# Kernel optimization log

Hardware: AMD Instinct MI355X
Metric: run time of the kernel (lower is better)

## Reference

```python
import jax, jax.numpy as jnp
import numpy as np

N = 10000          # nodes
E = 200000         # edges (avg degree 20)
LAT = 128          # latent dim
NEXP = 8           # experts
NTYPE = 95         # atom types (hard-coded 95x0e in module)
M0, M1, M2 = 128, 64, 32          # node/out irreps muls for l=0,1,2 (dim 480)
E0, E1, E2 = 64, 32, 16           # edge irreps muls (dim 240)
C0, C1, C2 = M0 + E0, M1 + E1, M2 + E2   # concat channels per l
T0 = M0 + M1 + M2                 # gate-input scalars: 128 scalars + 96 gates
AVG_NEIGH = 20.0


def setup_inputs() -> dict:
    key = jax.random.key(0)
    ks = jax.random.split(key, 32)
    r = lambda i, sh: jax.random.normal(ks[i], sh, dtype=jnp.float32)
    return {
        "latents": r(0, (E, LAT)),
        "node_features": r(1, (N, M0 + 3 * M1 + 5 * M2)),
        "edge_features": r(2, (E, E0 + 3 * E1 + 5 * E2)),
        "edge_vector": r(3, (E, 3)),
        "mole_globals": r(4, (LAT,)),
        "wigner_D1": r(5, (E, 3, 3)),
        "wigner_D2": r(6, (E, 5, 5)),
        "node_onehot": jax.nn.one_hot(jax.random.randint(ks[7], (N,), 0, NTYPE), NTYPE, dtype=jnp.float32),
        "Wg": r(8, (LAT, NEXP)),
        "Wm": r(9, (LAT, NEXP)),
        "W0_e": r(10, (NEXP, C0, T0)), "W0_s": r(11, (C0, T0)),
        "W1_e": r(12, (NEXP, C1, M1)), "W1_s": r(13, (C1, M1)),
        "W2_e": r(14, (NEXP, C2, M2)), "W2_s": r(15, (C2, M2)),
        "Wp0": r(16, (M0, M0)), "bp0": jnp.zeros((M0,), jnp.float32),
        "Wp1": r(17, (M1, M1)), "Wp2": r(18, (M2, M2)),
        "Wenv": r(19, (LAT, M0 + M1 + M2)),
        "Woh0": r(20, (M0, NTYPE)), "Woh1": r(21, (M1, NTYPE)), "Woh2": r(22, (M2, NTYPE)),
        "atom_type": jax.random.randint(ks[23], (N,), 0, NTYPE),
        "edge_index": jax.random.randint(ks[24], (2, E), 0, N),
        "active_edges": jnp.arange(E),
    }


def _mix(x, We, Ws, g):
    """Latent(expert)-conditioned per-l channel mixing: y = x @ (sum_e g_e W_e + W_shared).
    Loops over the small fixed expert count; never materializes per-edge weight matrices."""
    xm = x if x.ndim == 3 else x[:, :, None]           # [a, c, m]
    y = jnp.einsum('acm,co->aom', xm, Ws)
    for e in range(NEXP):
        y = y + g[:, e, None, None] * jnp.einsum('acm,co->aom', xm, We[e])
    y = y * float(1.0 / np.sqrt(xm.shape[1]))
    return y[:, :, 0] if x.ndim == 2 else y


def reference(latents, node_features, edge_features, edge_vector, mole_globals,
              wigner_D1, wigner_D2, node_onehot, Wg, Wm,
              W0_e, W0_s, W1_e, W1_s, W2_e, W2_s,
              Wp0, bp0, Wp1, Wp2, Wenv, Woh0, Woh1, Woh2,
              atom_type, edge_index, active_edges):
    edge_center = edge_index[0][active_edges]
    lat = latents[active_edges]
    # gather node features along edges, split irreps blocks
    xn = node_features[edge_center]                         # [Ea, 480]
    n0 = xn[:, :M0]
    n1 = xn[:, M0:M0 + 3 * M1].reshape(-1, M1, 3)
    n2 = xn[:, M0 + 3 * M1:].reshape(-1, M2, 5)
    e0 = edge_features[:, :E0]
    e1 = edge_features[:, E0:E0 + 3 * E1].reshape(-1, E1, 3)
    e2 = edge_features[:, E0 + 3 * E1:].reshape(-1, E2, 5)
    x0 = jnp.concatenate([n0, e0], axis=1)                  # [Ea, C0]
    x1 = jnp.concatenate([n1, e1], axis=1)                  # [Ea, C1, 3]
    x2 = jnp.concatenate([n2, e2], axis=1)                  # [Ea, C2, 5]
    # latent + molecular-global conditioned expert gates
    gates = jax.nn.softmax(lat @ Wg + mole_globals @ Wm, axis=-1)   # [Ea, NEXP]
    # SO(2)-style TP: rotate l>0 blocks into edge frame (Wigner-D), mix channels, rotate back
    x1r = jnp.einsum('amn,acn->acm', wigner_D1, x1)
    x2r = jnp.einsum('amn,acn->acm', wigner_D2, x2)
    t0 = _mix(x0, W0_e, W0_s, gates)                        # [Ea, T0]
    t1 = jnp.einsum('anm,aom->aon', wigner_D1, _mix(x1r, W1_e, W1_s, gates))
    t2 = jnp.einsum('anm,aom->aon', wigner_D2, _mix(x2r, W2_e, W2_s, gates))
    # Gate nonlinearity: silu scalars, sigmoid gates scale l>0 channels
    s = jax.nn.silu(t0[:, :M0])
    v1 = t1 * jax.nn.sigmoid(t0[:, M0:M0 + M1])[:, :, None]
    v2 = t2 * jax.nn.sigmoid(t0[:, M0 + M1:])[:, :, None]
    # lin_post: per-l equivariant linear (bias only on scalars), fan-in normalized
    s = s @ Wp0 * float(1.0 / np.sqrt(M0)) + bp0
    v1 = jnp.einsum('acm,co->aom', v1, Wp1) * float(1.0 / np.sqrt(M1))
    v2 = jnp.einsum('acm,co->aom', v2, Wp2) * float(1.0 / np.sqrt(M2))
    # E3ElementLinear: per-channel weights generated from latents
    w = lat @ Wenv * float(1.0 / np.sqrt(LAT))              # [Ea, M0+M1+M2]
    s = s * w[:, :M0]
    v1 = v1 * w[:, M0:M0 + M1, None]
    v2 = v2 * w[:, M0 + M1:, None]
    # scatter-reduce messages to nodes, normalize by rsqrt(avg_num_neighbors)
    norm = float(1.0 / np.sqrt(AVG_NEIGH))
    o0 = jax.ops.segment_sum(s, edge_center, num_segments=N) * norm
    o1 = jax.ops.segment_sum(v1, edge_center, num_segments=N) * norm
    o2 = jax.ops.segment_sum(v2, edge_center, num_segments=N) * norm
    # residual blend (res_update_params=0 -> u=sigmoid(0)=0.5), identity residual
    u = 0.5
    c_old = float(1.0 / np.sqrt(u * u + 1.0))
    c_new = u * c_old
    h0 = c_old * node_features[:, :M0] + c_new * o0
    h1 = c_old * node_features[:, M0:M0 + 3 * M1].reshape(N, M1, 3) + c_new * o1
    h2 = c_old * node_features[:, M0 + 3 * M1:].reshape(N, M2, 5) + c_new * o2
    # layer-onehot 'uvu' weighted TP with 95x0e, fan-in normalized, added residually
    invs = float(1.0 / np.sqrt(NTYPE))
    h0 = h0 + h0 * (node_onehot @ Woh0.T) * invs
    h1 = h1 + h1 * (node_onehot @ Woh1.T)[:, :, None] * invs
    h2 = h2 + h2 * (node_onehot @ Woh2.T)[:, :, None] * invs
    return jnp.concatenate([h0, h1.reshape(N, 3 * M1), h2.reshape(N, 5 * M2)], axis=1)
```

## Files before the change

### kernel.cpp

```cpp
#include <hip/hip_runtime.h>
#include <math.h>

namespace {

typedef __attribute__((ext_vector_type(8))) short short8;
typedef __attribute__((ext_vector_type(4))) float f32x4;

constexpr int kN   = 10000;
constexpr int kE   = 200000;
constexpr int kNT  = 95;
constexpr int kNFD = 480;

__device__ __forceinline__ ushort bf(float f) {
  union { float f; uint u; } c; c.f = f;
  uint r = c.u + 0x7FFF + ((c.u >> 16) & 1);
  return (ushort)(r >> 16);
}
__device__ __forceinline__ float fb(ushort u) {
  union { uint u; float f; } c; c.u = ((uint)u) << 16;
  return c.f;
}
__device__ __forceinline__ uint pk2(float a, float b) {
  return (uint)bf(a) | ((uint)bf(b) << 16);
}

__device__ __forceinline__ void packone(int u, const float* We, const float* Ws,
                                        int expStride, int Kreal, int Nstride,
                                        int Nreal, int NT, int NKp, ushort* d) {
  int i = u & 7;
  int lane = (u >> 3) & 63;
  int rest = u >> 9;
  int kc = rest % NKp; rest /= NKp;
  int nt = rest % NT;
  int e  = rest / NT;
  int k = kc*32 + (lane >> 4)*8 + i;
  int n = nt*16 + (lane & 15);
  float v = 0.f;
  if (k < Kreal && n < Nreal) {
    const float* s = (Ws != nullptr && e == 8) ? Ws : (We + (size_t)e*expStride);
    v = s[(size_t)k*Nstride + n];
  }
  d[u] = bf(v);
}

constexpr int PK0   = 0;
constexpr int PK1   = 442368;
constexpr int PK2   = 497664;
constexpr int PKENV = 516096;
constexpr int PKP0  = 544768;
constexpr int PKP1  = 561152;
constexpr int PKP2  = 565248;
constexpr int PKTOT = 566272;

__global__ __launch_bounds__(256)
void pack_k(const float* __restrict__ W0e, const float* __restrict__ W0s,
            const float* __restrict__ W1e, const float* __restrict__ W1s,
            const float* __restrict__ W2e, const float* __restrict__ W2s,
            const float* __restrict__ Wenv, const float* __restrict__ Wp0,
            const float* __restrict__ Wp1, const float* __restrict__ Wp2,
            ushort* __restrict__ dst) {
  int gid = blockIdx.x*256 + threadIdx.x;
  if (gid >= PKTOT) return;
  if (gid < PK1)        packone(gid - PK0,   W0e, W0s, 192*224, 192, 224, 224, 16, 6, dst + PK0);
  else if (gid < PK2)   packone(gid - PK1,   W1e, W1s, 96*64,    96,  64,  64,  4, 3, dst + PK1);
  else if (gid < PKENV) packone(gid - PK2,   W2e, W2s, 48*32,    48,  32,  32,  2, 2, dst + PK2);
  else if (gid < PKP0)  packone(gid - PKENV, Wenv, nullptr, 0,  128, 224, 224, 14, 4, dst + PKENV);
  else if (gid < PKP1)  packone(gid - PKP0,  Wp0, nullptr, 0,   128, 128, 128,  8, 4, dst + PKP0);
  else if (gid < PKP2)  packone(gid - PKP1,  Wp1, nullptr, 0,    64,  64,  64,  4, 2, dst + PKP1);
  else                  packone(gid - PKP2,  Wp2, nullptr, 0,    32,  32,  32,  2, 1, dst + PKP2);
}

__global__ __launch_bounds__(64)
void mgl_k(const float* __restrict__ mgv, const float* __restrict__ Wm,
           float* __restrict__ mgl) {
  int x = threadIdx.x;
  if (x < 8) {
    float s = 0.f;
    for (int l = 0; l < 128; ++l) s += mgv[l]*Wm[l*8 + x];
    mgl[x] = s;
  }
}

__global__ __launch_bounds__(256)
void hist_k(const int* __restrict__ eidx, const int* __restrict__ act,
            int* __restrict__ counts) {
  int e = blockIdx.x*256 + threadIdx.x;
  if (e < kE) atomicAdd(&counts[eidx[act[e]]], 1);
}

__global__ __launch_bounds__(256)
void scan_k(const int* __restrict__ counts, int* __restrict__ rowptr,
            int* __restrict__ cursor) {
  __shared__ int part[256];
  const int t = threadIdx.x;
  const int start = t*40;
  int local = 0;
  for (int i = 0; i < 40; ++i) {
    int idx = start + i;
    if (idx < kN) local += counts[idx];
  }
  part[t] = local;
  __syncthreads();
  for (int ofs = 1; ofs < 256; ofs <<= 1) {
    int v = (t >= ofs) ? part[t - ofs] : 0;
    __syncthreads();
    part[t] += v;
    __syncthreads();
  }
  int run = part[t] - local;
  for (int i = 0; i < 40; ++i) {
    int idx = start + i;
    if (idx < kN) {
      rowptr[idx] = run;
      cursor[idx] = run;
      run += counts[idx];
    }
  }
  if (t == 255) rowptr[kN] = run;
}

__global__ __launch_bounds__(256)
void scatter_k(const int* __restrict__ eidx, const int* __restrict__ act,
               int* __restrict__ cursor, int* __restrict__ elist) {
  int e = blockIdx.x*256 + threadIdx.x;
  if (e < kE) {
    int n = eidx[act[e]];
    int pos = atomicAdd(&cursor[n], 1);
    elist[pos] = e;
  }
}

__global__ __launch_bounds__(256)
void prep_k(const float* __restrict__ latents, const float* __restrict__ nodef,
            const float* __restrict__ edgef, const float* __restrict__ mgl,
            const float* __restrict__ D1, const float* __restrict__ D2,
            const float* __restrict__ Wg,
            const int* __restrict__ eidx, const int* __restrict__ act,
            float* __restrict__ coefg,
            ushort* __restrict__ x0, ushort* __restrict__ x1r,
            ushort* __restrict__ x2r) {
  __shared__ int aidl[32], cenl[32];
  const int tid = threadIdx.x;
  const int base = blockIdx.x*32;

  if (tid < 32) {
    int a = act[base + tid];
    aidl[tid] = a;
    cenl[tid] = eidx[a];
  }
  __syncthreads();

  {
    int e = tid >> 3, x = tid & 7;
    const float* lat = latents + (size_t)aidl[e]*128;
    float s = mgl[x];
    for (int l = 0; l < 128; ++l) s += lat[l]*Wg[l*8 + x];
    float mx = s;
    mx = fmaxf(mx, __shfl_xor(mx, 1));
    mx = fmaxf(mx, __shfl_xor(mx, 2));
    mx = fmaxf(mx, __shfl_xor(mx, 4));
    float ex = __expf(s - mx);
    float sm = ex;
    sm += __shfl_xor(sm, 1);
    sm += __shfl_xor(sm, 2);
    sm += __shfl_xor(sm, 4);
    size_t a = base + e;
    coefg[a*9 + x] = ex/sm;
    if (x == 0) coefg[a*9 + 8] = 1.f;
  }

  for (int u = tid; u < 32*24; u += 256) {
    int e = u/24, g = u - e*24;
    int c0 = g*8;
    size_t a = base + e;
    const float* s = (g < 16) ? (nodef + (size_t)cenl[e]*kNFD + c0)
                              : (edgef + a*240 + (c0 - 128));
    float4 f0 = *(const float4*)s;
    float4 f1 = *(const float4*)(s + 4);
    uint4 o;
    o.x = pk2(f0.x, f0.y); o.y = pk2(f0.z, f0.w);
    o.z = pk2(f1.x, f1.y); o.w = pk2(f1.z, f1.w);
    *(uint4*)(x0 + a*192 + c0) = o;
  }

  for (int u = tid; u < 32*36; u += 256) {
    int e = u/36, r = u - e*36;
    int mm = r/12, g = r - mm*12;
    int c0 = g*8;
    size_t a = base + e;
    const float* dd = D1 + a*9 + mm*3;
    const float* s = (g < 8) ? (nodef + (size_t)cenl[e]*kNFD + 128 + c0*3)
                             : (edgef + a*240 + 64 + (c0 - 64)*3);
    float ld[24];
    #pragma unroll
    for (int q = 0; q < 6; ++q)
      *(float4*)(ld + q*4) = *(const float4*)(s + q*4);
    float d0 = dd[0], d1 = dd[1], d2 = dd[2];
    float ov[8];
    #pragma unroll
    for (int j = 0; j < 8; ++j)
      ov[j] = d0*ld[3*j] + d1*ld[3*j + 1] + d2*ld[3*j + 2];
    uint4 o;
    o.x = pk2(ov[0], ov[1]); o.y = pk2(ov[2], ov[3]);
    o.z = pk2(ov[4], ov[5]); o.w = pk2(ov[6], ov[7]);
    *(uint4*)(x1r + (a*3 + mm)*96 + c0) = o;
  }

  for (int u = tid; u < 32*40; u += 256) {
    int e = u/40, r = u - e*40;
    int mm = r >> 3, g = r & 7;
    int c0 = g*8;
    size_t a = base + e;
    uint4 o = {0u,0u,0u,0u};
    if (g < 6) {
      const float* dd = D2 + a*25 + mm*5;
      const float* s = (g < 4) ? (nodef + (size_t)cenl[e]*kNFD + 320 + c0*5)
                               : (edgef + a*240 + 160 + (c0 - 32)*5);
      float ld[40];
      #pragma unroll
      for (int q = 0; q < 10; ++q)
        *(float4*)(ld + q*4) = *(const float4*)(s + q*4);
      float d0 = dd[0], d1 = dd[1], d2 = dd[2], d3 = dd[3], d4 = dd[4];
      float ov[8];
      #pragma unroll
      for (int j = 0; j < 8; ++j)
        ov[j] = d0*ld[5*j] + d1*ld[5*j+1] + d2*ld[5*j+2] + d3*ld[5*j+3] + d4*ld[5*j+4];
      o.x = pk2(ov[0], ov[1]); o.y = pk2(ov[2], ov[3]);
      o.z = pk2(ov[4], ov[5]); o.w = pk2(ov[6], ov[7]);
    }
    *(uint4*)(x2r + (a*5 + mm)*64 + c0) = o;
  }
}

constexpr int gemm_smbytes(int K1, int NK, int N, int NEXP) {
  int LDA = K1 + 8;
  int NT = N/16;
  int a = 128*LDA*2;
  int b = NT*NK*1024;
  int u = a > b ? a : b;
  return u + (NEXP > 1 ? 128*NEXP*4 : 0);
}

template<int DIV, int K1, int NK, int N, int NEXP, int EPI, bool AF32>
__global__ __launch_bounds__(512)
void gemm_k(const ushort* __restrict__ A, const float* __restrict__ Af,
            const int* __restrict__ ridx, int strideA,
            const ushort* __restrict__ Bpk, const float* __restrict__ coefg,
            int rowsReal, float norm,
            ushort* __restrict__ outbf, const float* __restrict__ bias,
            const ushort* __restrict__ wenvbf, int WCOL) {
  constexpr int NT  = N/16;
  constexpr int CTW = NT/2;
  constexpr int LDA = K1 + 8;
  constexpr int ABYTES = 128*LDA*2;
  constexpr int BBYTES = NT*NK*1024;
  constexpr int UNI = (ABYTES > BBYTES) ? ABYTES : BBYTES;

  extern __shared__ char smraw[];
  ushort* Asm = (ushort*)smraw;
  float* coefsm = (float*)(smraw + UNI);

  const int tid = threadIdx.x;
  const int row0 = blockIdx.x*128;

  constexpr int C8 = K1/8;
  for (int u = tid; u < 128*C8; u += 512) {
    int r = u / C8, c8 = u - r*C8;
    int gr = row0 + r;
    uint4 v = {0u,0u,0u,0u};
    if (gr < rowsReal) {
      if constexpr (AF32) {
        const float* s = Af + (size_t)(ridx ? ridx[gr] : gr)*strideA + c8*8;
        float4 f0 = *(const float4*)s;
        float4 f1 = *(const float4*)(s + 4);
        v.x = pk2(f0.x, f0.y); v.y = pk2(f0.z, f0.w);
        v.z = pk2(f1.x, f1.y); v.w = pk2(f1.z, f1.w);
      } else {
        v = *(const uint4*)(A + (size_t)gr*strideA + c8*8);
      }
    }
    *(uint4*)(&Asm[r*LDA + c8*8]) = v;
  }
  if constexpr (NEXP > 1) {
    for (int u = tid; u < 128*NEXP; u += 512) {
      int r = u / NEXP, e = u - r*NEXP;
      int a = (row0 + r)/DIV;
      coefsm[r*NEXP + e] = coefg[(size_t)a*NEXP + e];
    }
  }
  __syncthreads();

  const int lane = tid & 63, wid = tid >> 6;
  const int cg = wid & 1, rg = wid >> 1;
  const int rbase = rg*32;
  const int lrow = lane & 15, lkb = lane >> 4;

  short8 af[2][NK];
  #pragma unroll
  for (int rt = 0; rt < 2; ++rt)
    #pragma unroll
    for (int kc = 0; kc < NK; ++kc)
      af[rt][kc] = *(const short8*)(&Asm[(rbase + rt*16 + lrow)*LDA + kc*32 + lkb*8]);

  f32x4 acc[2][CTW];
  #pragma unroll
  for (int rt = 0; rt < 2; ++rt)
    #pragma unroll
    for (int ct = 0; ct < CTW; ++ct)
      acc[rt][ct] = f32x4{0.f,0.f,0.f,0.f};

  __syncthreads();

  union BU { uint4 u; short8 s; };
  uint4* Bsm4 = (uint4*)smraw;
  const uint4* Bg4 = (const uint4*)Bpk;

  for (int e = 0; e < NEXP; ++e) {
    for (int u = tid; u < NT*NK*64; u += 512)
      Bsm4[u] = Bg4[(size_t)e*(NT*NK*64) + u];
    __syncthreads();

    if constexpr (NEXP > 1) {
      float cf[2][4];
      #pragma unroll
      for (int rt = 0; rt < 2; ++rt)
        #pragma unroll
        for (int q = 0; q < 4; ++q)
          cf[rt][q] = coefsm[(rbase + rt*16 + lkb*4 + q)*NEXP + e];
      #pragma unroll
      for (int ct = 0; ct < CTW; ++ct) {
        int nt = cg*CTW + ct;
        f32x4 z[2];
        z[0] = f32x4{0.f,0.f,0.f,0.f};
        z[1] = f32x4{0.f,0.f,0.f,0.f};
        #pragma unroll
        for (int kc = 0; kc < NK; ++kc) {
          BU b; b.u = Bsm4[(nt*NK + kc)*64 + lane];
          z[0] = __builtin_amdgcn_mfma_f32_16x16x32_bf16(af[0][kc], b.s, z[0], 0, 0, 0);
          z[1] = __builtin_amdgcn_mfma_f32_16x16x32_bf16(af[1][kc], b.s, z[1], 0, 0, 0);
        }
        #pragma unroll
        for (int q = 0; q < 4; ++q) {
          acc[0][ct][q] += cf[0][q]*z[0][q];
          acc[1][ct][q] += cf[1][q]*z[1][q];
        }
      }
    } else {
      #pragma unroll
      for (int ct = 0; ct < CTW; ++ct) {
        int nt = cg*CTW + ct;
        #pragma unroll
        for (int kc = 0; kc < NK; ++kc) {
          BU b; b.u = Bsm4[(nt*NK + kc)*64 + lane];
          acc[0][ct] = __builtin_amdgcn_mfma_f32_16x16x32_bf16(af[0][kc], b.s, acc[0][ct], 0, 0, 0);
          acc[1][ct] = __builtin_amdgcn_mfma_f32_16x16x32_bf16(af[1][kc], b.s, acc[1][ct], 0, 0, 0);
        }
      }
    }
    __syncthreads();
  }

  #pragma unroll
  for (int rt = 0; rt < 2; ++rt) {
    #pragma unroll
    for (int ct = 0; ct < CTW; ++ct) {
      #pragma unroll
      for (int q = 0; q < 4; ++q) {
        int gr = row0 + rbase + rt*16 + lkb*4 + q;
        if (gr >= rowsReal) continue;
        int o = (cg*CTW + ct)*16 + lrow;
        float val = acc[rt][ct][q]*norm;
        if constexpr (EPI == 0) {
          outbf[(size_t)gr*N + o] = bf(val);
        } else if constexpr (EPI == 1) {
          float av = (o < 128) ? (val/(1.f + __expf(-val)))
                               : (1.f/(1.f + __expf(-val)));
          outbf[(size_t)gr*N + o] = bf(av);
        } else {
          int a = gr/DIV;
          if (bias != nullptr) val += bias[o];
          float w = fb(wenvbf[(size_t)a*224 + WCOL + o]);
          val *= w*0.22360679774997896f;
          outbf[(size_t)gr*N + o] = bf(val);
        }
      }
    }
  }
}

constexpr int T0SMB = 55808;

template<int C>
__device__ __forceinline__ void t0_phase(int e, int tid, int lane, int cg,
                                         int rbase, int lkb,
                                         const short8 (&af)[2][6],
                                         f32x4 (&acc)[2][7],
                                         const float* coefsm,
                                         uint4* Bsm4, const uint4* Bg4,
                                         uint4& rg0, uint4& rg1, uint4& rg2) {
  __syncthreads();
  const bool hasNext = !(e == 8 && C == 3);
  if (hasNext) {
    int ne = e + (C == 3 ? 1 : 0);
    int nc = (C + 1) & 3;
    const uint4* s = Bg4 + (size_t)ne*6144 + (size_t)nc*1536;
    rg0 = s[tid]; rg1 = s[tid + 512]; rg2 = s[tid + 1024];
  }
  float cf[2][4];
  #pragma unroll
  for (int rt = 0; rt < 2; ++rt)
    #pragma unroll
    for (int q = 0; q < 4; ++q)
      cf[rt][q] = coefsm[(rbase + rt*16 + lkb*4 + q)*9 + e];
  union BU { uint4 u; short8 s; };
  const uint4* bb = Bsm4 + (C & 1)*1536;
  {
    f32x4 z0 = {0.f,0.f,0.f,0.f}, z1 = {0.f,0.f,0.f,0.f};
    #pragma unroll
    for (int kc = 0; kc < 6; ++kc) {
      BU b; b.u = bb[(cg*6 + kc)*64 + lane];
      z0 = __builtin_amdgcn_mfma_f32_16x16x32_bf16(af[0][kc], b.s, z0, 0, 0, 0);
      z1 = __builtin_amdgcn_mfma_f32_16x16x32_bf16(af[1][kc], b.s, z1, 0, 0, 0);
    }
    #pragma unroll
    for (int q = 0; q < 4; ++q) {
      acc[0][2*C][q] += cf[0][q]*z0[q];
      acc[1][2*C][q] += cf[1][q]*z1[q];
    }
  }
  if constexpr (2*C + 1 < 7) {
    f32x4 z0 = {0.f,0.f,0.f,0.f}, z1 = {0.f,0.f,0.f,0.f};
    #pragma unroll
    for (int kc = 0; kc < 6; ++kc) {
      BU b; b.u = bb[((2 + cg)*6 + kc)*64 + lane];
      z0 = __builtin_amdgcn_mfma_f32_16x16x32_bf16(af[0][kc], b.s, z0, 0, 0, 0);
      z1 = __builtin_amdgcn_mfma_f32_16x16x32_bf16(af[1][kc], b.s, z1, 0, 0, 0);
    }
    #pragma unroll
    for (int q = 0; q < 4; ++q) {
      acc[0][2*C + 1][q] += cf[0][q]*z0[q];
      acc[1][2*C + 1][q] += cf[1][q]*z1[q];
    }
  }
  __syncthreads();
  if (hasNext) {
    uint4* d = Bsm4 + ((C + 1) & 1)*1536;
    d[tid] = rg0; d[tid + 512] = rg1; d[tid + 1024] = rg2;
  }
}

__global__ __launch_bounds__(512, 2)
void t0c_k(const ushort* __restrict__ A, const ushort* __restrict__ Bpk,
           const float* __restrict__ coefg, ushort* __restrict__ outbf) {
  extern __shared__ char smraw[];
  ushort* Asm = (ushort*)smraw;
  float* coefsm = (float*)(smraw + 51200);
  uint4* Bsm4 = (uint4*)smraw;
  const uint4* Bg4 = (const uint4*)Bpk;

  const int tid = threadIdx.x;
  const int row0 = blockIdx.x*128;

  for (int u = tid; u < 128*24; u += 512) {
    int r = u/24, c8 = u - r*24;
    int gr = row0 + r;
    uint4 v = {0u,0u,0u,0u};
    if (gr < kE) v = *(const uint4*)(A + (size_t)gr*192 + c8*8);
    *(uint4*)(&Asm[r*200 + c8*8]) = v;
  }
  for (int u = tid; u < 128*9; u += 512) {
    int r = u/9, e = u - r*9;
    coefsm[r*9 + e] = coefg[(size_t)(row0 + r)*9 + e];
  }
  __syncthreads();

  const int lane = tid & 63, wid = tid >> 6;
  const int cg = wid & 1, rg = wid >> 1;
  const int rbase = rg*32;
  const int lrow = lane & 15, lkb = lane >> 4;

  short8 af[2][6];
  #pragma unroll
  for (int rt = 0; rt < 2; ++rt)
    #pragma unroll
    for (int kc = 0; kc < 6; ++kc)
      af[rt][kc] = *(const short8*)(&Asm[(rbase + rt*16 + lrow)*200 + kc*32 + lkb*8]);

  f32x4 acc[2][7];
  #pragma unroll
  for (int rt = 0; rt < 2; ++rt)
    #pragma unroll
    for (int ct = 0; ct < 7; ++ct)
      acc[rt][ct] = f32x4{0.f,0.f,0.f,0.f};

  __syncthreads();

  uint4 rg0, rg1, rg2;
  { const uint4* s = Bg4; rg0 = s[tid]; rg1 = s[tid + 512]; rg2 = s[tid + 1024]; }
  { uint4* d = Bsm4;      d[tid] = rg0; d[tid + 512] = rg1; d[tid + 1024] = rg2; }

  for (int e = 0; e < 9; ++e) {
    t0_phase<0>(e, tid, lane, cg, rbase, lkb, af, acc, coefsm, Bsm4, Bg4, rg0, rg1, rg2);
    t0_phase<1>(e, tid, lane, cg, rbase, lkb, af, acc, coefsm, Bsm4, Bg4, rg0, rg1, rg2);
    t0_phase<2>(e, tid, lane, cg, rbase, lkb, af, acc, coefsm, Bsm4, Bg4, rg0, rg1, rg2);
    t0_phase<3>(e, tid, lane, cg, rbase, lkb, af, acc, coefsm, Bsm4, Bg4, rg0, rg1, rg2);
  }

  #pragma unroll
  for (int rt = 0; rt < 2; ++rt) {
    #pragma unroll
    for (int ct = 0; ct < 7; ++ct) {
      #pragma unroll
      for (int q = 0; q < 4; ++q) {
        int gr = row0 + rbase + rt*16 + lkb*4 + q;
        if (gr >= kE) continue;
        int o = (2*ct + cg)*16 + lrow;
        float val = acc[rt][ct][q]*0.07216878364870323f;
        float av = (o < 128) ? (val/(1.f + __expf(-val)))
                             : (1.f/(1.f + __expf(-val)));
        outbf[(size_t)gr*224 + o] = bf(av);
      }
    }
  }
}

__global__ __launch_bounds__(256)
void mid_k(const ushort* __restrict__ y1, const ushort* __restrict__ y2,
           const ushort* __restrict__ t0act, const float* __restrict__ D1,
           const float* __restrict__ D2, ushort* __restrict__ v1,
           ushort* __restrict__ v2) {
  const int base = blockIdx.x*64;
  const int tid = threadIdx.x;

  for (int u = tid; u < 64*24; u += 256) {
    int e = u/24, r = u - e*24;
    int n = r >> 3, g = r & 7;
    int c0 = g*8;
    size_t a = base + e;
    const float* dd = D1 + a*9 + n*3;
    float d0 = dd[0], d1 = dd[1], d2 = dd[2];
    short8 m0 = *(const short8*)(y1 + ((size_t)a*3 + 0)*64 + c0);
    short8 m1 = *(const short8*)(y1 + ((size_t)a*3 + 1)*64 + c0);
    short8 m2 = *(const short8*)(y1 + ((size_t)a*3 + 2)*64 + c0);
    short8 gt = *(const short8*)(t0act + a*224 + 128 + c0);
    float ov[8];
    #pragma unroll
    for (int j = 0; j < 8; ++j) {
      float s = d0*fb((ushort)m0[j]) + d1*fb((ushort)m1[j]) + d2*fb((ushort)m2[j]);
      ov[j] = s*fb((ushort)gt[j]);
    }
    uint4 o;
    o.x = pk2(ov[0], ov[1]); o.y = pk2(ov[2], ov[3]);
    o.z = pk2(ov[4], ov[5]); o.w = pk2(ov[6], ov[7]);
    *(uint4*)(v1 + ((size_t)a*3 + n)*64 + c0) = o;
  }

  for (int u = tid; u < 64*20; u += 256) {
    int e = u/20, r = u - e*20;
    int n = r >> 2, g = r & 3;
    int c0 = g*8;
    size_t a = base + e;
    const float* dd = D2 + a*25 + n*5;
    short8 m0 = *(const short8*)(y2 + ((size_t)a*5 + 0)*32 + c0);
    short8 m1 = *(const short8*)(y2 + ((size_t)a*5 + 1)*32 + c0);
    short8 m2 = *(const short8*)(y2 + ((size_t)a*5 + 2)*32 + c0);
    short8 m3 = *(const short8*)(y2 + ((size_t)a*5 + 3)*32 + c0);
    short8 m4 = *(const short8*)(y2 + ((size_t)a*5 + 4)*32 + c0);
    short8 gt = *(const short8*)(t0act + a*224 + 192 + c0);
    float ov[8];
    #pragma unroll
    for (int j = 0; j < 8; ++j) {
      float s = dd[0]*fb((ushort)m0[j]) + dd[1]*fb((ushort)m1[j])
              + dd[2]*fb((ushort)m2[j]) + dd[3]*fb((ushort)m3[j])
              + dd[4]*fb((ushort)m4[j]);
      ov[j] = s*fb((ushort)gt[j]);
    }
    uint4 o;
    o.x = pk2(ov[0], ov[1]); o.y = pk2(ov[2], ov[3]);
    o.z = pk2(ov[4], ov[5]); o.w = pk2(ov[6], ov[7]);
    *(uint4*)(v2 + ((size_t)a*5 + n)*32 + c0) = o;
  }
}

__global__ __launch_bounds__(256)
void gather_k(const float* __restrict__ nodef, const float* __restrict__ onehot,
              const float* __restrict__ Woh0, const float* __restrict__ Woh1,
              const float* __restrict__ Woh2,
              const int* __restrict__ rowptr, const int* __restrict__ elist,
              const ushort* __restrict__ pe0, const ushort* __restrict__ pe1,
              const ushort* __restrict__ pe2, float* __restrict__ out) {
  __shared__ int tn;
  const int n = blockIdx.x;
  const int t = threadIdx.x;
  if (t < kNT && onehot[(size_t)n*kNT + t] > 0.5f) tn = t;
  __syncthreads();
  const int ty = tn;
  const int r0 = rowptr[n], r1 = rowptr[n + 1];
  const float c_old = 0.8944271909999159f;
  const float c_new = 0.4472135954999579f;
  const float invs  = 0.10259783520851541f;

  for (int j = t; j < kNFD; j += 256) {
    int kind, row_m, col;
    if (j < 128)       { kind = 0; row_m = 0; col = j; }
    else if (j < 320)  { int jj = j - 128; col = jj/3; row_m = jj - col*3; kind = 1; }
    else               { int jj = j - 320; col = jj/5; row_m = jj - col*5; kind = 2; }

    float s = 0.f;
    for (int d = r0; d < r1; ++d) {
      int e = elist[d];
      ushort v;
      if (kind == 0)      v = pe0[(size_t)e*128 + col];
      else if (kind == 1) v = pe1[((size_t)e*3 + row_m)*64 + col];
      else                v = pe2[((size_t)e*5 + row_m)*32 + col];
      s += fb(v);
    }

    size_t idx = (size_t)n*kNFD + j;
    float h = c_old*nodef[idx] + c_new*s;
    float f;
    if (j < 128)      f = Woh0[j*kNT + ty];
    else if (j < 320) f = Woh1[((j - 128)/3)*kNT + ty];
    else              f = Woh2[((j - 320)/5)*kNT + ty];
    out[idx] = h*(1.f + f*invs);
  }
}

constexpr size_t OFF_CNT  = 0;
constexpr size_t OFF_CUR  = 40000;
constexpr size_t OFF_RP   = 80000;
constexpr size_t OFF_EL   = 120064;
constexpr size_t OFF_PACK = 1000000;
constexpr size_t OFF_COEF = 19200000;
constexpr size_t OFF_MGL  = 26402304;
constexpr size_t OFF_X0   = 27202560;
constexpr size_t OFF_X1R  = 104027136;
constexpr size_t OFF_X2R  = 219264000;
constexpr size_t OFF_WENV = 347272192;
constexpr size_t OFF_T0A  = 436900864;
constexpr size_t OFF_Y1   = 526529536;
constexpr size_t OFF_Y2   = 603354112;

}

extern "C" void kernel_launch(void* const* d_in, const int* in_sizes, int n_in,
                              void* d_out, int out_size, void* d_ws, size_t ws_size,
                              hipStream_t stream) {
  (void)in_sizes; (void)n_in; (void)out_size; (void)ws_size;
  const float* latents = (const float*)d_in[0];
  const float* nodef   = (const float*)d_in[1];
  const float* edgef   = (const float*)d_in[2];
  const float* mg      = (const float*)d_in[4];
  const float* D1      = (const float*)d_in[5];
  const float* D2      = (const float*)d_in[6];
  const float* onehot  = (const float*)d_in[7];
  const float* Wg      = (const float*)d_in[8];
  const float* Wm      = (const float*)d_in[9];
  const float* W0e     = (const float*)d_in[10];
  const float* W0s     = (const float*)d_in[11];
  const float* W1e     = (const float*)d_in[12];
  const float* W1s     = (const float*)d_in[13];
  const float* W2e     = (const float*)d_in[14];
  const float* W2s     = (const float*)d_in[15];
  const float* Wp0     = (const float*)d_in[16];
  const float* bp0     = (const float*)d_in[17];
  const float* Wp1     = (const float*)d_in[18];
  const float* Wp2     = (const float*)d_in[19];
  const float* Wenv    = (const float*)d_in[20];
  const float* Woh0    = (const float*)d_in[21];
  const float* Woh1    = (const float*)d_in[22];
  const float* Woh2    = (const float*)d_in[23];
  const int* eidx      = (const int*)d_in[25];
  const int* act       = (const int*)d_in[26];

  char* ws = (char*)d_ws;
  int*    cnt   = (int*)(ws + OFF_CNT);
  int*    cur   = (int*)(ws + OFF_CUR);
  int*    rp    = (int*)(ws + OFF_RP);
  int*    el    = (int*)(ws + OFF_EL);
  ushort* pk    = (ushort*)(ws + OFF_PACK);
  float*  coef  = (float*)(ws + OFF_COEF);
  float*  mgl   = (float*)(ws + OFF_MGL);
  ushort* x0    = (ushort*)(ws + OFF_X0);
  ushort* x1r   = (ushort*)(ws + OFF_X1R);
  ushort* x2r   = (ushort*)(ws + OFF_X2R);
  ushort* wenv  = (ushort*)(ws + OFF_WENV);
  ushort* t0act = (ushort*)(ws + OFF_T0A);
  ushort* y1    = (ushort*)(ws + OFF_Y1);
  ushort* y2    = (ushort*)(ws + OFF_Y2);
  ushort* v1    = (ushort*)(ws + OFF_X0);
  ushort* v2    = (ushort*)(ws + OFF_X1R);
  ushort* pe1   = (ushort*)(ws + OFF_X2R);
  ushort* pe2   = (ushort*)(ws + OFF_Y1);
  ushort* pe0   = (ushort*)(ws + OFF_Y2);
  float*  out   = (float*)d_out;

  hipMemsetAsync(cnt, 0, kN*sizeof(int), stream);
  hist_k<<<(kE + 255)/256, 256, 0, stream>>>(eidx, act, cnt);
  scan_k<<<1, 256, 0, stream>>>(cnt, rp, cur);
  scatter_k<<<(kE + 255)/256, 256, 0, stream>>>(eidx, act, cur, el);

  pack_k<<<(PKTOT + 255)/256, 256, 0, stream>>>(W0e, W0s, W1e, W1s, W2e, W2s,
                                                Wenv, Wp0, Wp1, Wp2, pk);
  mgl_k<<<1, 64, 0, stream>>>(mg, Wm, mgl);

  prep_k<<<kE/32, 256, 0, stream>>>(latents, nodef, edgef, mgl, D1, D2, Wg,
                                    eidx, act, coef, x0, x1r, x2r);

  {
    hipFuncSetAttribute((const void*)t0c_k,
                        hipFuncAttributeMaxDynamicSharedMemorySize, T0SMB);
    t0c_k<<<1563, 512, T0SMB, stream>>>(x0, pk + PK0, coef, t0act);
  }
  {
    auto kp = gemm_k<1,128,4,224,1,0,true>;
    int smb = gemm_smbytes(128,4,224,1);
    hipFuncSetAttribute((const void*)kp, hipFuncAttributeMaxDynamicSharedMemorySize, smb);
    kp<<<1563, 512, smb, stream>>>(
        nullptr, latents, act, 128, pk + PKENV, nullptr, kE, 0.08838834764831845f,
        wenv, nullptr, nullptr, 0);
  }
  {
    auto kp = gemm_k<3,96,3,64,9,0,false>;
    int smb = gemm_smbytes(96,3,64,9);
    hipFuncSetAttribute((const void*)kp, hipFuncAttributeMaxDynamicSharedMemorySize, smb);
    kp<<<4688, 512, smb, stream>>>(
        x1r, nullptr, nullptr, 96, pk + PK1, coef, 3*kE, 0.10206207261596577f,
        y1, nullptr, nullptr, 0);
  }
  {
    auto kp = gemm_k<5,64,2,32,9,0,false>;
    int smb = gemm_smbytes(64,2,32,9);
    hipFuncSetAttribute((const void*)kp, hipFuncAttributeMaxDynamicSharedMemorySize, smb);
    kp<<<7813, 512, smb, stream>>>(
        x2r, nullptr, nullptr, 64, pk + PK2, coef, 5*kE, 0.14433756729740643f,
        y2, nullptr, nullptr, 0);
  }

  mid_k<<<kE/64, 256, 0, stream>>>(y1, y2, t0act, D1, D2, v1, v2);

  {
    auto kp = gemm_k<1,128,4,128,1,2,false>;
    int smb = gemm_smbytes(128,4,128,1);
    hipFuncSetAttribute((const void*)kp, hipFuncAttributeMaxDynamicSharedMemorySize, smb);
    kp<<<1563, 512, smb, stream>>>(
        t0act, nullptr, nullptr, 224, pk + PKP0, nullptr, kE, 0.08838834764831845f,
        pe0, bp0, wenv, 0);
  }
  {
    auto kp = gemm_k<3,64,2,64,1,2,false>;
    int smb = gemm_smbytes(64,2,64,1);
    hipFuncSetAttribute((const void*)kp, hipFuncAttributeMaxDynamicSharedMemorySize, smb);
    kp<<<4688, 512, smb, stream>>>(
        v1, nullptr, nullptr, 64, pk + PKP1, nullptr, 3*kE, 0.125f,
        pe1, nullptr, wenv, 128);
  }
  {
    auto kp = gemm_k<5,32,1,32,1,2,false>;
    int smb = gemm_smbytes(32,1,32,1);
    hipFuncSetAttribute((const void*)kp, hipFuncAttributeMaxDynamicSharedMemorySize, smb);
    kp<<<7813, 512, smb, stream>>>(
        v2, nullptr, nullptr, 32, pk + PKP2, nullptr, 5*kE, 0.17677669529663687f,
        pe2, nullptr, wenv, 192);
  }

  gather_k<<<kN, 256, 0, stream>>>(nodef, onehot, Woh0, Woh1, Woh2,
                                   rp, el, pe0, pe1, pe2, out);
}
```

Measured before the change: 1.434 ms.

## Add dedicated double-buffered expert-mixing GEMM kernel for l=1,2 and lighter barriers

Replaces the generic gemm_k launches for the l=1 and l=2 expert-mixing GEMMs with a specialized kernel. It keeps A fragments in registers, streams each expert's packed weights through a double-buffered LDS with register prefetch, and accumulates coefficient-scaled MFMA results. It also swaps __syncthreads for a barrier that waits only on LDS counters (lgkmcnt) in both this kernel and the t0 kernel. The aim is to cut generic-kernel overhead and barrier stalls. The risk is that global prefetch loads are not covered by the barrier's wait.

```diff
diff --git a/kernel.cpp b/kernel.cpp
--- a/kernel.cpp
+++ b/kernel.cpp
@@ -22,6 +22,11 @@
 }
 __device__ __forceinline__ uint pk2(float a, float b) {
   return (uint)bf(a) | ((uint)bf(b) << 16);
+}
+
+__device__ __forceinline__ void fastbar() {
+  asm volatile("s_waitcnt lgkmcnt(0)" ::: "memory");
+  __builtin_amdgcn_s_barrier();
 }
 
 __device__ __forceinline__ void packone(int u, const float* We, const float* Ws,
@@ -398,7 +403,7 @@
                                          const float* coefsm,
                                          uint4* Bsm4, const uint4* Bg4,
                                          uint4& rg0, uint4& rg1, uint4& rg2) {
-  __syncthreads();
+  fastbar();
   const bool hasNext = !(e == 8 && C == 3);
   if (hasNext) {
     int ne = e + (C == 3 ? 1 : 0);
@@ -442,7 +447,7 @@
       acc[1][2*C + 1][q] += cf[1][q]*z1[q];
     }
   }
-  __syncthreads();
+  fastbar();
   if (hasNext) {
     uint4* d = Bsm4 + ((C + 1) & 1)*1536;
     d[tid] = rg0; d[tid + 512] = rg1; d[tid + 1024] = rg2;
@@ -519,6 +524,132 @@
         float av = (o < 128) ? (val/(1.f + __expf(-val)))
                              : (1.f/(1.f + __expf(-val)));
         outbf[(size_t)gr*224 + o] = bf(av);
+      }
+    }
+  }
+}
+
+constexpr int ych_smbytes(int K1, int NK, int NT) {
+  int a = 128*(K1 + 8)*2;
+  int b = 2*NT*NK*1024;
+  int u = a > b ? a : b;
+  return u + 128*9*4;
+}
+
+template<int DIV, int K1, int NK, int NT>
+__global__ __launch_bounds__(512, 2)
+void ychunk_k(const ushort* __restrict__ A, const ushort* __restrict__ Bpk,
+              const float* __restrict__ coefg, int rowsReal, float norm,
+              ushort* __restrict__ outbf) {
+  constexpr int CTW = NT/2;
+  constexpr int N   = NT*16;
+  constexpr int LDA = K1 + 8;
+  constexpr int ABYTES = 128*LDA*2;
+  constexpr int BBYTES = 2*NT*NK*1024;
+  constexpr int UNI = (ABYTES > BBYTES) ? ABYTES : BBYTES;
+  constexpr int NB4 = NT*NK*64;
+
+  extern __shared__ char smraw[];
+  ushort* Asm = (ushort*)smraw;
+  float* coefsm = (float*)(smraw + UNI);
+  uint4* Bsm4 = (uint4*)smraw;
+  const uint4* Bg4 = (const uint4*)Bpk;
+
+  const int tid = threadIdx.x;
+  const int row0 = blockIdx.x*128;
+
+  constexpr int C8 = K1/8;
+  for (int u = tid; u < 128*C8; u += 512) {
+    int r = u / C8, c8 = u - r*C8;
+    int gr = row0 + r;
+    uint4 v = {0u,0u,0u,0u};
+    if (gr < rowsReal) v = *(const uint4*)(A + (size_t)gr*K1 + c8*8);
+    *(uint4*)(&Asm[r*LDA + c8*8]) = v;
+  }
+  for (int u = tid; u < 128*9; u += 512) {
+    int r = u/9, e = u - r*9;
+    int a = (row0 + r)/DIV;
+    coefsm[r*9 + e] = coefg[(size_t)a*9 + e];
+  }
+  __syncthreads();
+
+  const int lane = tid & 63, wid = tid >> 6;
+  const int cg = wid & 1, rg = wid >> 1;
+  const int rbase = rg*32;
+  const int lrow = lane & 15, lkb = lane >> 4;
+
+  short8 af[2][NK];
+  #pragma unroll
+  for (int rt = 0; rt < 2; ++rt)
+    #pragma unroll
+    for (int kc = 0; kc < NK; ++kc)
+      af[rt][kc] = *(const short8*)(&Asm[(rbase + rt*16 + lrow)*LDA + kc*32 + lkb*8]);
+
+  f32x4 acc[2][CTW];
+  #pragma unroll
+  for (int rt = 0; rt < 2; ++rt)
+    #pragma unroll
+    for (int ct = 0; ct < CTW; ++ct)
+      acc[rt][ct] = f32x4{0.f,0.f,0.f,0.f};
+
+  __syncthreads();
+
+  union BU { uint4 u; short8 s; };
+  uint4 pf0, pf1;
+
+  if (tid < NB4) pf0 = Bg4[tid];
+  if constexpr (NB4 > 512) { if (tid + 512 < NB4) pf1 = Bg4[tid + 512]; }
+  if (tid < NB4) Bsm4[tid] = pf0;
+  if constexpr (NB4 > 512) { if (tid + 512 < NB4) Bsm4[tid + 512] = pf1; }
+
+  for (int e = 0; e < 9; ++e) {
+    fastbar();
+    if (e + 1 < 9) {
+      const uint4* s = Bg4 + (size_t)(e + 1)*NB4;
+      if (tid < NB4) pf0 = s[tid];
+      if constexpr (NB4 > 512) { if (tid + 512 < NB4) pf1 = s[tid + 512]; }
+    }
+    float cf[2][4];
+    #pragma unroll
+    for (int rt = 0; rt < 2; ++rt)
+      #pragma unroll
+      for (int q = 0; q < 4; ++q)
+        cf[rt][q] = coefsm[(rbase + rt*16 + lkb*4 + q)*9 + e];
+    const uint4* bb = Bsm4 + (e & 1)*NB4;
+    #pragma unroll
+    for (int ct = 0; ct < CTW; ++ct) {
+      int nt = cg*CTW + ct;
+      f32x4 z0 = {0.f,0.f,0.f,0.f}, z1 = {0.f,0.f,0.f,0.f};
+      #pragma unroll
+      for (int kc = 0; kc < NK; ++kc) {
+        BU b; b.u = bb[(nt*NK + kc)*64 + lane];
+        z0 = __builtin_amdgcn_mfma_f32_16x16x32_bf16(af[0][kc], b.s, z0, 0, 0, 0);
+        z1 = __builtin_amdgcn_mfma_f32_16x16x32_bf16(af[1][kc], b.s, z1, 0, 0, 0);
+      }
+      #pragma unroll
+      for (int q = 0; q < 4; ++q) {
+        acc[0][ct][q] += cf[0][q]*z0[q];
+        acc[1][ct][q] += cf[1][q]*z1[q];
+      }
+    }
+    fastbar();
+    if (e + 1 < 9) {
+      uint4* d = Bsm4 + ((e + 1) & 1)*NB4;
+      if (tid < NB4) d[tid] = pf0;
+      if constexpr (NB4 > 512) { if (tid + 512 < NB4) d[tid + 512] = pf1; }
+    }
+  }
+
+  #pragma unroll
+  for (int rt = 0; rt < 2; ++rt) {
+    #pragma unroll
+    for (int ct = 0; ct < CTW; ++ct) {
+      #pragma unroll
+      for (int q = 0; q < 4; ++q) {
+        int gr = row0 + rbase + rt*16 + lkb*4 + q;
+        if (gr >= rowsReal) continue;
+        int o = (cg*CTW + ct)*16 + lrow;
+        outbf[(size_t)gr*N + o] = bf(acc[rt][ct][q]*norm);
       }
     }
   }
@@ -721,20 +852,18 @@
         wenv, nullptr, nullptr, 0);
   }
   {
-    auto kp = gemm_k<3,96,3,64,9,0,false>;
-    int smb = gemm_smbytes(96,3,64,9);
+    auto kp = ychunk_k<3,96,3,4>;
+    int smb = ych_smbytes(96,3,4);
     hipFuncSetAttribute((const void*)kp, hipFuncAttributeMaxDynamicSharedMemorySize, smb);
     kp<<<4688, 512, smb, stream>>>(
-        x1r, nullptr, nullptr, 96, pk + PK1, coef, 3*kE, 0.10206207261596577f,
-        y1, nullptr, nullptr, 0);
+        x1r, pk + PK1, coef, 3*kE, 0.10206207261596577f, y1);
   }
   {
-    auto kp = gemm_k<5,64,2,32,9,0,false>;
-    int smb = gemm_smbytes(64,2,32,9);
+    auto kp = ychunk_k<5,64,2,2>;
+    int smb = ych_smbytes(64,2,2);
     hipFuncSetAttribute((const void*)kp, hipFuncAttributeMaxDynamicSharedMemorySize, smb);
     kp<<<7813, 512, smb, stream>>>(
-        x2r, nullptr, nullptr, 64, pk + PK2, coef, 5*kE, 0.14433756729740643f,
-        y2, nullptr, nullptr, 0);
+        x2r, pk + PK2, coef, 5*kE, 0.14433756729740643f, y2);
   }
 
   mid_k<<<kE/64, 256, 0, stream>>>(y1, y2, t0act, D1, D2, v1, v2);
```

After: 1.381 ms. 3.7% less time.
